# Performance work log

Measured on AMD Instinct MI355X. Metric: run time of the kernel, lower is better.

Reference implementation:

```python
import jax, jax.numpy as jnp
import numpy as np

N_NODES = 8192
N_EDGES = 65536
IN_DIM = 768
HIDDEN = 4096
N_CLASSES = 16


def setup_inputs() -> dict:
    key = jax.random.key(0)
    k1, k2, k3, k4 = jax.random.split(key, 4)
    x = jax.random.normal(k1, (N_NODES, IN_DIM), dtype=jnp.float32)
    edge_index = jax.random.randint(k2, (2, N_EDGES), 0, N_NODES, dtype=jnp.int64)
    # Glorot-ish init scale
    W1 = jax.random.normal(k3, (IN_DIM, HIDDEN), dtype=jnp.float32) * (1.0 / np.sqrt(IN_DIM))
    b1 = jnp.zeros((HIDDEN,), dtype=jnp.float32)
    W2 = jax.random.normal(k4, (HIDDEN, N_CLASSES), dtype=jnp.float32) * (1.0 / np.sqrt(HIDDEN))
    b2 = jnp.zeros((N_CLASSES,), dtype=jnp.float32)
    return {"x": x, "edge_index": edge_index, "W1": W1, "b1": b1, "W2": W2, "b2": b2}


def reference(x, edge_index, W1, b1, W2, b2):
    # GCNConv (PyG defaults): add self-loops, symmetric deg^-1/2 normalization,
    # transform-then-aggregate, plus bias. Then ReLU -> (dropout=identity at
    # inference) -> Linear -> log_softmax.
    N = x.shape[0]
    loops = jnp.arange(N, dtype=edge_index.dtype)
    src = jnp.concatenate([edge_index[0], loops])  # [E+N]
    dst = jnp.concatenate([edge_index[1], loops])  # [E+N]

    h = x @ W1  # [N, HIDDEN] dense GEMM

    deg = jax.ops.segment_sum(jnp.ones_like(dst, dtype=h.dtype), dst, num_segments=N)
    dinv = jnp.where(deg > 0, jax.lax.rsqrt(jnp.maximum(deg, 1e-12)), 0.0)
    norm = dinv[src] * dinv[dst]  # [E+N]

    agg = jax.ops.segment_sum(h[src] * norm[:, None], dst, num_segments=N)  # [N, HIDDEN]
    h = jax.nn.relu(agg + b1)

    logits = h @ W2 + b2  # [N, N_CLASSES]
    return jax.nn.log_softmax(logits, axis=1)
```

## Files before the change

kernel.cpp:

```cpp
#include <hip/hip_runtime.h>

#define N_NODES   8192
#define N_EDGES   65536
#define IN_DIM    768
#define HIDDEN    4096
#define N_CLASSES 16
#define SLOTS     64
#define NSLAB     16

typedef unsigned short ushort_t;
typedef __attribute__((ext_vector_type(8))) short bf16x8;
typedef __attribute__((ext_vector_type(4))) float f32x4;

__device__ __forceinline__ ushort_t f2bf(float f) {
    union { float f; unsigned i; } v; v.f = f;
    unsigned r = v.i + 0x7FFFu + ((v.i >> 16) & 1u);
    return (ushort_t)(r >> 16);
}
__device__ __forceinline__ float bf2f(ushort_t u) {
    union { unsigned i; float f; } v; v.i = ((unsigned)u) << 16; return v.f;
}

#define GLD_LDS16(gp, lp) \
    __builtin_amdgcn_global_load_lds((const __attribute__((address_space(1))) void*)(gp), \
                                     (__attribute__((address_space(3))) void*)(lp), 16, 0, 0)

__device__ __forceinline__ int esrc(const int* ei, int f32mode, int e) {
    return f32mode ? ei[e] : ei[2 * e];
}
__device__ __forceinline__ int edst(const int* ei, int f32mode, int e) {
    return f32mode ? ei[N_EDGES + e] : ei[2 * N_EDGES + 2 * e];
}

__global__ __launch_bounds__(256) void phase1(const float* __restrict__ x,
                                              ushort_t* __restrict__ xbf,
                                              const float* __restrict__ W2,
                                              ushort_t* __restrict__ W2T,
                                              const int* __restrict__ ei,
                                              int* __restrict__ cnt,
                                              int* __restrict__ slots,
                                              int* __restrict__ flag) {
    int b = blockIdx.x, t = threadIdx.x;
    if (b < 16) {
        __shared__ ushort_t ld[16 * 257];
        int k0 = b * 256;
        const float4* src = (const float4*)(W2 + (long)(k0 + t) * N_CLASSES);
        #pragma unroll
        for (int j = 0; j < 4; j++) {
            float4 v = src[j];
            ld[(j * 4 + 0) * 257 + t] = f2bf(v.x);
            ld[(j * 4 + 1) * 257 + t] = f2bf(v.y);
            ld[(j * 4 + 2) * 257 + t] = f2bf(v.z);
            ld[(j * 4 + 3) * 257 + t] = f2bf(v.w);
        }
        __syncthreads();
        #pragma unroll
        for (int c = 0; c < 16; c++)
            W2T[c * HIDDEN + k0 + t] = ld[c * 257 + t];
    } else if (b < 1552) {
        long i = (long)(b - 16) * 1024 + t;
        #pragma unroll
        for (int p = 0; p < 4; p++) {
            float4 v = ((const float4*)x)[i + p * 256];
            ushort4 r = { f2bf(v.x), f2bf(v.y), f2bf(v.z), f2bf(v.w) };
            ((ushort4*)xbf)[i + p * 256] = r;
        }
    } else {
        __shared__ int sv[256];
        int v = 0;
        for (int e = t; e < 4096; e += 256) v |= ei[2 * e + 1];
        sv[t] = v;
        __syncthreads();
        for (int off = 128; off > 0; off >>= 1) {
            if (t < off) sv[t] |= sv[t + off];
            __syncthreads();
        }
        int f = (sv[0] != 0) ? 1 : 0;
        if (b == 1552 && t == 0) *flag = f;
        int e = (b - 1552) * 256 + t;
        int s = esrc(ei, f, e), d = edst(ei, f, e);
        int p = atomicAdd(&cnt[d], 1);
        if (p < SLOTS) slots[d * SLOTS + p] = s;
    }
}

__global__ __launch_bounds__(256) void phase2(const float* __restrict__ W1,
                                              ushort_t* __restrict__ W1T,
                                              const ushort_t* __restrict__ xbf,
                                              const int* __restrict__ cnt,
                                              const int* __restrict__ slots,
                                              const int* __restrict__ ei,
                                              const int* __restrict__ flag,
                                              ushort_t* __restrict__ xagg) {
    int b = blockIdx.x, t = threadIdx.x;
    if (b < 3072) {
        __shared__ ushort_t tile[32][33];
        int n0 = (b & 127) * 32, k0 = (b >> 7) * 32;
        int tx = t & 31, ty = t >> 5;
        #pragma unroll
        for (int j = 0; j < 4; j++) {
            int k = ty * 4 + j;
            tile[k][tx] = f2bf(W1[(k0 + k) * HIDDEN + n0 + tx]);
        }
        __syncthreads();
        #pragma unroll
        for (int j = 0; j < 4; j++) {
            int n = ty * 4 + j;
            W1T[(n0 + n) * IN_DIM + k0 + tx] = tile[tx][n];
        }
        return;
    }
    if (t >= 192) return;
    int w = t >> 6, l = t & 63;
    int d = b - 3072;
    int fo = w * 256 + l * 4;
    int cd = cnt[d];
    float wd = rsqrtf((float)(cd + 1));
    ushort4 sv = *(const ushort4*)(xbf + (long)d * IN_DIM + fo);
    float a0 = wd * bf2f(sv.x), a1 = wd * bf2f(sv.y);
    float a2 = wd * bf2f(sv.z), a3 = wd * bf2f(sv.w);

    if (cd <= SLOTS) {
        const int* sl = slots + d * SLOTS;
        int j = 0;
        for (; j + 4 <= cd; j += 4) {
            int s0 = sl[j], s1 = sl[j + 1], s2 = sl[j + 2], s3 = sl[j + 3];
            float w0 = rsqrtf((float)(cnt[s0] + 1));
            float w1 = rsqrtf((float)(cnt[s1] + 1));
            float w2 = rsqrtf((float)(cnt[s2] + 1));
            float w3 = rsqrtf((float)(cnt[s3] + 1));
            ushort4 v0 = *(const ushort4*)(xbf + (long)s0 * IN_DIM + fo);
            ushort4 v1 = *(const ushort4*)(xbf + (long)s1 * IN_DIM + fo);
            ushort4 v2 = *(const ushort4*)(xbf + (long)s2 * IN_DIM + fo);
            ushort4 v3 = *(const ushort4*)(xbf + (long)s3 * IN_DIM + fo);
            a0 = fmaf(w0, bf2f(v0.x), a0); a1 = fmaf(w0, bf2f(v0.y), a1);
            a2 = fmaf(w0, bf2f(v0.z), a2); a3 = fmaf(w0, bf2f(v0.w), a3);
            a0 = fmaf(w1, bf2f(v1.x), a0); a1 = fmaf(w1, bf2f(v1.y), a1);
            a2 = fmaf(w1, bf2f(v1.z), a2); a3 = fmaf(w1, bf2f(v1.w), a3);
            a0 = fmaf(w2, bf2f(v2.x), a0); a1 = fmaf(w2, bf2f(v2.y), a1);
            a2 = fmaf(w2, bf2f(v2.z), a2); a3 = fmaf(w2, bf2f(v2.w), a3);
            a0 = fmaf(w3, bf2f(v3.x), a0); a1 = fmaf(w3, bf2f(v3.y), a1);
            a2 = fmaf(w3, bf2f(v3.z), a2); a3 = fmaf(w3, bf2f(v3.w), a3);
        }
        for (; j < cd; j++) {
            int s = sl[j];
            float ws = rsqrtf((float)(cnt[s] + 1));
            ushort4 v = *(const ushort4*)(xbf + (long)s * IN_DIM + fo);
            a0 = fmaf(ws, bf2f(v.x), a0); a1 = fmaf(ws, bf2f(v.y), a1);
            a2 = fmaf(ws, bf2f(v.z), a2); a3 = fmaf(ws, bf2f(v.w), a3);
        }
    } else {
        int f = *flag;
        for (int e = 0; e < N_EDGES; e++) {
            if (edst(ei, f, e) == d) {
                int s = esrc(ei, f, e);
                float ws = rsqrtf((float)(cnt[s] + 1));
                ushort4 v = *(const ushort4*)(xbf + (long)s * IN_DIM + fo);
                a0 = fmaf(ws, bf2f(v.x), a0); a1 = fmaf(ws, bf2f(v.y), a1);
                a2 = fmaf(ws, bf2f(v.z), a2); a3 = fmaf(ws, bf2f(v.w), a3);
            }
        }
    }
    ushort4 r = { f2bf(a0 * wd), f2bf(a1 * wd), f2bf(a2 * wd), f2bf(a3 * wd) };
    *(ushort4*)(xagg + (long)d * IN_DIM + fo) = r;
}

#define FENCE() asm volatile("" ::: "memory")
#define BAR()  do { FENCE(); __builtin_amdgcn_s_barrier(); FENCE(); } while (0)
#define VMCNT(n) asm volatile("s_waitcnt vmcnt(" #n ")" ::: "memory")
#define LGKM0()  asm volatile("s_waitcnt lgkmcnt(0)" ::: "memory")
#define PRIO(x)  __builtin_amdgcn_s_setprio(x)

__global__ __launch_bounds__(512, 2) void gemm1_fused(const ushort_t* __restrict__ A,
                                                      const ushort_t* __restrict__ Bt,
                                                      const float* __restrict__ b1,
                                                      const ushort_t* __restrict__ W2T,
                                                      float* __restrict__ part) {
    __shared__ ushort_t lds[65536];
    ushort_t* ldsA = lds;
    ushort_t* ldsB = lds + 32768;

    int t = threadIdx.x;
    int w = t >> 6, l = t & 63;
    int wm = w & 3, wn = w >> 2;
    int q = l >> 4, lm = l & 15;
    int bx = blockIdx.x & 15, by = blockIdx.x >> 4;
    int m0 = by * 256, n0 = bx * 256;

    int srow = t >> 3;
    int sg = (t & 7) ^ (srow & 7);
    const ushort_t* aS = A  + (long)(m0 + srow) * IN_DIM + sg * 8;
    const ushort_t* bS = Bt + (long)(n0 + srow) * IN_DIM + sg * 8;

#define STAGE_A(B_, h, ko) do { \
    GLD_LDS16(aS + (h) * 128 * IN_DIM + (ko),              ldsA + (B_) * 16384 + (h) * 8192 + w * 512); \
    GLD_LDS16(aS + ((h) * 128 + 64) * IN_DIM + (ko),       ldsA + (B_) * 16384 + (h) * 8192 + 4096 + w * 512); \
} while (0)
#define STAGE_B(B_, h, ko) do { \
    GLD_LDS16(bS + (h) * 128 * IN_DIM + (ko),              ldsB + (B_) * 16384 + (h) * 8192 + w * 512); \
    GLD_LDS16(bS + ((h) * 128 + 64) * IN_DIM + (ko),       ldsB + (B_) * 16384 + (h) * 8192 + 4096 + w * 512); \
} while (0)
#define LDA(dst, qm, B_) do { \
    const ushort_t* p_ = ldsA + (B_) * 16384 + (wm * 64 + (qm) * 32 + lm) * 64; \
    int x0_ = ((q) ^ (lm & 7)) * 8, x1_ = ((4 + q) ^ (lm & 7)) * 8; \
    dst[0][0] = *(const bf16x8*)(p_ + x0_);        dst[0][1] = *(const bf16x8*)(p_ + x1_); \
    dst[1][0] = *(const bf16x8*)(p_ + 1024 + x0_); dst[1][1] = *(const bf16x8*)(p_ + 1024 + x1_); \
} while (0)
#define LDB(dst, qn, B_) do { \
    const ushort_t* p_ = ldsB + (B_) * 16384 + (wn * 128 + (qn) * 64 + lm) * 64; \
    int x0_ = ((q) ^ (lm & 7)) * 8, x1_ = ((4 + q) ^ (lm & 7)) * 8; \
    dst[0][0] = *(const bf16x8*)(p_ + x0_);        dst[0][1] = *(const bf16x8*)(p_ + x1_); \
    dst[1][0] = *(const bf16x8*)(p_ + 1024 + x0_); dst[1][1] = *(const bf16x8*)(p_ + 1024 + x1_); \
    dst[2][0] = *(const bf16x8*)(p_ + 2048 + x0_); dst[2][1] = *(const bf16x8*)(p_ + 2048 + x1_); \
    dst[3][0] = *(const bf16x8*)(p_ + 3072 + x0_); dst[3][1] = *(const bf16x8*)(p_ + 3072 + x1_); \
} while (0)
#define MFMAQ(qm, qn, a_, b_) do { \
    _Pragma("unroll") for (int j_ = 0; j_ < 2; j_++) \
    _Pragma("unroll") for (int nt_ = 0; nt_ < 4; nt_++) \
    _Pragma("unroll") for (int mt_ = 0; mt_ < 2; mt_++) \
        acc[(qm) * 2 + mt_][(qn) * 4 + nt_] = __builtin_amdgcn_mfma_f32_16x16x32_bf16( \
            a_[mt_][j_], b_[nt_][j_], acc[(qm) * 2 + mt_][(qn) * 4 + nt_], 0, 0, 0); \
} while (0)

    int kA = 0, kB = 0;
    STAGE_A(0, 0, kA); STAGE_A(0, 1, kA); kA += 64;
    STAGE_B(0, 0, kB); STAGE_B(0, 1, kB); kB += 64;
    STAGE_A(1, 0, kA); STAGE_A(1, 1, kA); kA += 64;

    bf16x8 aq0[2][2], aq1[2][2], bq0[4][2], bq1[4][2];
    f32x4 acc[4][8] = {};

    VMCNT(4);
    BAR();

    #pragma unroll 1
    for (int it = 0; it < 5; ++it) {
        LDA(aq0, 0, 0); LDB(bq0, 0, 0); STAGE_B(1, 0, kB);
        BAR(); LGKM0(); PRIO(1); MFMAQ(0, 0, aq0, bq0); PRIO(0); BAR();
        LDA(aq1, 1, 0); STAGE_B(1, 1, kB); kB += 64;
        BAR(); LGKM0(); PRIO(1); MFMAQ(1, 0, aq1, bq0); PRIO(0); BAR();
        LDB(bq1, 1, 0); STAGE_A(0, 0, kA);
        BAR(); LGKM0(); PRIO(1); MFMAQ(1, 1, aq1, bq1); PRIO(0); BAR();
        STAGE_A(0, 1, kA); kA += 64;
        VMCNT(4);
        BAR(); PRIO(1); MFMAQ(0, 1, aq0, bq1); PRIO(0); BAR();
        LDA(aq0, 0, 1); LDB(bq0, 0, 1); STAGE_B(0, 0, kB);
        BAR(); LGKM0(); PRIO(1); MFMAQ(0, 0, aq0, bq0); PRIO(0); BAR();
        LDA(aq1, 1, 1); STAGE_B(0, 1, kB); kB += 64;
        BAR(); LGKM0(); PRIO(1); MFMAQ(1, 0, aq1, bq0); PRIO(0); BAR();
        LDB(bq1, 1, 1); STAGE_A(1, 0, kA);
        BAR(); LGKM0(); PRIO(1); MFMAQ(1, 1, aq1, bq1); PRIO(0); BAR();
        STAGE_A(1, 1, kA); kA += 64;
        VMCNT(4);
        BAR(); PRIO(1); MFMAQ(0, 1, aq0, bq1); PRIO(0); BAR();
    }
    LDA(aq0, 0, 0); LDB(bq0, 0, 0); STAGE_B(1, 0, kB);
    BAR(); LGKM0(); PRIO(1); MFMAQ(0, 0, aq0, bq0); PRIO(0); BAR();
    LDA(aq1, 1, 0); STAGE_B(1, 1, kB);
    BAR(); LGKM0(); PRIO(1); MFMAQ(1, 0, aq1, bq0); PRIO(0); BAR();
    LDB(bq1, 1, 0);
    BAR(); LGKM0(); PRIO(1); MFMAQ(1, 1, aq1, bq1); PRIO(0); BAR();
    VMCNT(0);
    BAR(); PRIO(1); MFMAQ(0, 1, aq0, bq1); PRIO(0); BAR();
    LDA(aq0, 0, 1); LDB(bq0, 0, 1);
    BAR(); LGKM0(); PRIO(1); MFMAQ(0, 0, aq0, bq0); PRIO(0); BAR();
    LDA(aq1, 1, 1);
    BAR(); LGKM0(); PRIO(1); MFMAQ(1, 0, aq1, bq0); PRIO(0); BAR();
    LDB(bq1, 1, 1);
    BAR(); LGKM0(); PRIO(1); MFMAQ(1, 1, aq1, bq1); PRIO(0); BAR();
    PRIO(1); MFMAQ(0, 1, aq0, bq1); PRIO(0);

    float bias[8];
    #pragma unroll
    for (int ng = 0; ng < 8; ng++) bias[ng] = b1[n0 + wn * 128 + ng * 16 + lm];
    bf16x8 w2f[2][2];
    #pragma unroll
    for (int eh = 0; eh < 2; eh++)
        #pragma unroll
        for (int kk = 0; kk < 2; kk++)
            w2f[eh][kk] = *(const bf16x8*)(W2T + (long)lm * HIDDEN + n0 + wn * 128 + eh * 64 + kk * 32 + q * 8);

    __syncthreads();
    ushort_t* slab = lds + w * 4096;
    f32x4 acc2[4] = {};
    #pragma unroll
    for (int eh = 0; eh < 2; eh++) {
        #pragma unroll
        for (int mg = 0; mg < 4; mg++)
            #pragma unroll
            for (int nt = 0; nt < 4; nt++) {
                int gc = nt * 2 + (lm >> 3);
                #pragma unroll
                for (int rr = 0; rr < 4; rr++) {
                    int row = mg * 16 + q * 4 + rr;
                    float v = acc[mg][eh * 4 + nt][rr] + bias[eh * 4 + nt];
                    v = v > 0.0f ? v : 0.0f;
                    slab[row * 64 + ((gc ^ (row & 7)) * 8) + (lm & 7)] = f2bf(v);
                }
            }
        #pragma unroll
        for (int kk = 0; kk < 2; kk++)
            #pragma unroll
            for (int mt2 = 0; mt2 < 4; mt2++) {
                bf16x8 a2 = *(const bf16x8*)(slab + (mt2 * 16 + lm) * 64 + (((kk * 4 + q) ^ (lm & 7)) * 8));
                acc2[mt2] = __builtin_amdgcn_mfma_f32_16x16x32_bf16(a2, w2f[eh][kk], acc2[mt2], 0, 0, 0);
            }
    }

    __syncthreads();
    float* psum = (float*)lds;
    if (wn == 1) {
        #pragma unroll
        for (int mt2 = 0; mt2 < 4; mt2++)
            #pragma unroll
            for (int rr = 0; rr < 4; rr++)
                psum[(wm * 64 + mt2 * 16 + q * 4 + rr) * 17 + lm] = acc2[mt2][rr];
    }
    __syncthreads();
    if (wn == 0) {
        float* pslab = part + ((long)bx * N_NODES + m0 + wm * 64) * N_CLASSES;
        #pragma unroll
        for (int mt2 = 0; mt2 < 4; mt2++)
            #pragma unroll
            for (int rr = 0; rr < 4; rr++) {
                int row = mt2 * 16 + q * 4 + rr;
                pslab[row * N_CLASSES + lm] = acc2[mt2][rr] + psum[(wm * 64 + row) * 17 + lm];
            }
    }
#undef STAGE_A
#undef STAGE_B
#undef LDA
#undef LDB
#undef MFMAQ
}

__global__ __launch_bounds__(256) void reduce_softmax(const float* __restrict__ part,
                                                      const float* __restrict__ b2,
                                                      float* __restrict__ out) {
    int t = threadIdx.x;
    int row = blockIdx.x * 16 + (t >> 4);
    int cls = t & 15;
    float v = b2[cls];
    #pragma unroll
    for (int s = 0; s < NSLAB; s++)
        v += part[((long)s * N_NODES + row) * N_CLASSES + cls];
    float mx = v;
    #pragma unroll
    for (int off = 1; off < 16; off <<= 1)
        mx = fmaxf(mx, __shfl_xor(mx, off, 64));
    float e = __expf(v - mx);
    float sm = e;
    #pragma unroll
    for (int off = 1; off < 16; off <<= 1)
        sm += __shfl_xor(sm, off, 64);
    out[(long)row * N_CLASSES + cls] = v - mx - __logf(sm);
}


extern "C" void kernel_launch(void* const* d_in, const int* in_sizes, int n_in,
                              void* d_out, int out_size, void* d_ws, size_t ws_size,
                              hipStream_t stream) {
    const float* x  = (const float*)d_in[0];
    const int*   ei = (const int*)d_in[1];
    const float* W1 = (const float*)d_in[2];
    const float* b1 = (const float*)d_in[3];
    const float* W2 = (const float*)d_in[4];
    const float* b2 = (const float*)d_in[5];
    float* out = (float*)d_out;
    char* ws = (char*)d_ws;

    float*    part  = (float*)(ws);
    ushort_t* xagg  = (ushort_t*)(ws + 16777216);
    ushort_t* xbf   = (ushort_t*)(ws + 29360128);
    ushort_t* W1T   = (ushort_t*)(ws + 41943040);
    ushort_t* W2T   = (ushort_t*)(ws + 48234496);
    int*      cnt   = (int*)(ws + 48365568);
    int*      slots = (int*)(ws + 48398336);
    int*      flag  = (int*)(ws + 50495488);

    hipMemsetAsync(cnt, 0, 32768, stream);
    phase1<<<1808, 256, 0, stream>>>(x, xbf, W2, W2T, ei, cnt, slots, flag);
    phase2<<<11264, 256, 0, stream>>>(W1, W1T, xbf, cnt, slots, ei, flag, xagg);
    gemm1_fused<<<(N_NODES / 256) * (HIDDEN / 256), 512, 0, stream>>>(xagg, W1T, b1, W2T, part);
    reduce_softmax<<<N_NODES / 16, 256, 0, stream>>>(part, b2, out);
}
```

Baseline: 159.7 us.

## Move W1 transpose into phase1 and remap gather to one node per wave

Moves the W1 fp32-to-bf16 transpose blocks from phase2 into phase1, so phase2 only does the neighbour aggregation. Phase2 now gives each wave its own destination node and spreads the three 256-feature slices across separate grid passes, which uses all four waves per block instead of idling the fourth. The gather loop is unrolled to 8 neighbours so more independent loads are in flight. The cost is more divergence between waves in a block, since neighbouring nodes have different degrees, and more registers for the deeper unroll.

```diff
diff --git a/kernel.cpp b/kernel.cpp
--- a/kernel.cpp
+++ b/kernel.cpp
@@ -34,6 +34,8 @@
 
 __global__ __launch_bounds__(256) void phase1(const float* __restrict__ x,
                                               ushort_t* __restrict__ xbf,
+                                              const float* __restrict__ W1,
+                                              ushort_t* __restrict__ W1T,
                                               const float* __restrict__ W2,
                                               ushort_t* __restrict__ W2T,
                                               const int* __restrict__ ei,
@@ -65,7 +67,7 @@
             ushort4 r = { f2bf(v.x), f2bf(v.y), f2bf(v.z), f2bf(v.w) };
             ((ushort4*)xbf)[i + p * 256] = r;
         }
-    } else {
+    } else if (b < 1808) {
         __shared__ int sv[256];
         int v = 0;
         for (int e = t; e < 4096; e += 256) v |= ei[2 * e + 1];
@@ -81,83 +83,80 @@
         int s = esrc(ei, f, e), d = edst(ei, f, e);
         int p = atomicAdd(&cnt[d], 1);
         if (p < SLOTS) slots[d * SLOTS + p] = s;
-    }
-}
-
-__global__ __launch_bounds__(256) void phase2(const float* __restrict__ W1,
-                                              ushort_t* __restrict__ W1T,
-                                              const ushort_t* __restrict__ xbf,
+    } else {
+        __shared__ ushort_t tile[32][33];
+        int bt = b - 1808;
+        int n0 = (bt & 127) * 32, k0 = (bt >> 7) * 32;
+        int tx = t & 31, ty = t >> 5;
+        #pragma unroll
+        for (int j = 0; j < 4; j++) {
+            int k = ty * 4 + j;
+            tile[k][tx] = f2bf(W1[(k0 + k) * HIDDEN + n0 + tx]);
+        }
+        __syncthreads();
+        #pragma unroll
+        for (int j = 0; j < 4; j++) {
+            int n = ty * 4 + j;
+            W1T[(n0 + n) * IN_DIM + k0 + tx] = tile[tx][n];
+        }
+    }
+}
+
+__global__ __launch_bounds__(256) void phase2(const ushort_t* __restrict__ xbf,
                                               const int* __restrict__ cnt,
                                               const int* __restrict__ slots,
                                               const int* __restrict__ ei,
                                               const int* __restrict__ flag,
                                               ushort_t* __restrict__ xagg) {
-    int b = blockIdx.x, t = threadIdx.x;
-    if (b < 3072) {
-        __shared__ ushort_t tile[32][33];
-        int n0 = (b & 127) * 32, k0 = (b >> 7) * 32;
-        int tx = t & 31, ty = t >> 5;
-        #pragma unroll
-        for (int j = 0; j < 4; j++) {
-            int k = ty * 4 + j;
-            tile[k][tx] = f2bf(W1[(k0 + k) * HIDDEN + n0 + tx]);
-        }
-        __syncthreads();
-        #pragma unroll
-        for (int j = 0; j < 4; j++) {
-            int n = ty * 4 + j;
-            W1T[(n0 + n) * IN_DIM + k0 + tx] = tile[tx][n];
-        }
-        return;
-    }
-    if (t >= 192) return;
+    int t = threadIdx.x;
     int w = t >> 6, l = t & 63;
-    int d = b - 3072;
-    int fo = w * 256 + l * 4;
+    int b = blockIdx.x;
+    int pass = b >> 11;
+    int d = (b & 2047) * 4 + w;
+    int fo = pass * 256 + l * 4;
     int cd = cnt[d];
     float wd = rsqrtf((float)(cd + 1));
-    ushort4 sv = *(const ushort4*)(xbf + (long)d * IN_DIM + fo);
-    float a0 = wd * bf2f(sv.x), a1 = wd * bf2f(sv.y);
-    float a2 = wd * bf2f(sv.z), a3 = wd * bf2f(sv.w);
-
+    float a0, a1, a2, a3;
+    {
+        ushort4 v = *(const ushort4*)(xbf + (long)d * IN_DIM + fo);
+        a0 = wd * bf2f(v.x); a1 = wd * bf2f(v.y);
+        a2 = wd * bf2f(v.z); a3 = wd * bf2f(v.w);
+    }
     if (cd <= SLOTS) {
         const int* sl = slots + d * SLOTS;
         int j = 0;
-        for (; j + 4 <= cd; j += 4) {
-            int s0 = sl[j], s1 = sl[j + 1], s2 = sl[j + 2], s3 = sl[j + 3];
-            float w0 = rsqrtf((float)(cnt[s0] + 1));
-            float w1 = rsqrtf((float)(cnt[s1] + 1));
-            float w2 = rsqrtf((float)(cnt[s2] + 1));
-            float w3 = rsqrtf((float)(cnt[s3] + 1));
-            ushort4 v0 = *(const ushort4*)(xbf + (long)s0 * IN_DIM + fo);
-            ushort4 v1 = *(const ushort4*)(xbf + (long)s1 * IN_DIM + fo);
-            ushort4 v2 = *(const ushort4*)(xbf + (long)s2 * IN_DIM + fo);
-            ushort4 v3 = *(const ushort4*)(xbf + (long)s3 * IN_DIM + fo);
-            a0 = fmaf(w0, bf2f(v0.x), a0); a1 = fmaf(w0, bf2f(v0.y), a1);
-            a2 = fmaf(w0, bf2f(v0.z), a2); a3 = fmaf(w0, bf2f(v0.w), a3);
-            a0 = fmaf(w1, bf2f(v1.x), a0); a1 = fmaf(w1, bf2f(v1.y), a1);
-            a2 = fmaf(w1, bf2f(v1.z), a2); a3 = fmaf(w1, bf2f(v1.w), a3);
-            a0 = fmaf(w2, bf2f(v2.x), a0); a1 = fmaf(w2, bf2f(v2.y), a1);
-            a2 = fmaf(w2, bf2f(v2.z), a2); a3 = fmaf(w2, bf2f(v2.w), a3);
-            a0 = fmaf(w3, bf2f(v3.x), a0); a1 = fmaf(w3, bf2f(v3.y), a1);
-            a2 = fmaf(w3, bf2f(v3.z), a2); a3 = fmaf(w3, bf2f(v3.w), a3);
+        for (; j + 8 <= cd; j += 8) {
+            int s[8]; float ws[8]; ushort4 v[8];
+            #pragma unroll
+            for (int k = 0; k < 8; k++) s[k] = sl[j + k];
+            #pragma unroll
+            for (int k = 0; k < 8; k++) ws[k] = rsqrtf((float)(cnt[s[k]] + 1));
+            #pragma unroll
+            for (int k = 0; k < 8; k++) v[k] = *(const ushort4*)(xbf + (long)s[k] * IN_DIM + fo);
+            #pragma unroll
+            for (int k = 0; k < 8; k++) {
+                a0 = fmaf(ws[k], bf2f(v[k].x), a0);
+                a1 = fmaf(ws[k], bf2f(v[k].y), a1);
+                a2 = fmaf(ws[k], bf2f(v[k].z), a2);
+                a3 = fmaf(ws[k], bf2f(v[k].w), a3);
+            }
         }
         for (; j < cd; j++) {
             int s = sl[j];
-            float ws = rsqrtf((float)(cnt[s] + 1));
+            float wsv = rsqrtf((float)(cnt[s] + 1));
             ushort4 v = *(const ushort4*)(xbf + (long)s * IN_DIM + fo);
-            a0 = fmaf(ws, bf2f(v.x), a0); a1 = fmaf(ws, bf2f(v.y), a1);
-            a2 = fmaf(ws, bf2f(v.z), a2); a3 = fmaf(ws, bf2f(v.w), a3);
+            a0 = fmaf(wsv, bf2f(v.x), a0); a1 = fmaf(wsv, bf2f(v.y), a1);
+            a2 = fmaf(wsv, bf2f(v.z), a2); a3 = fmaf(wsv, bf2f(v.w), a3);
         }
     } else {
         int f = *flag;
         for (int e = 0; e < N_EDGES; e++) {
             if (edst(ei, f, e) == d) {
                 int s = esrc(ei, f, e);
-                float ws = rsqrtf((float)(cnt[s] + 1));
+                float wsv = rsqrtf((float)(cnt[s] + 1));
                 ushort4 v = *(const ushort4*)(xbf + (long)s * IN_DIM + fo);
-                a0 = fmaf(ws, bf2f(v.x), a0); a1 = fmaf(ws, bf2f(v.y), a1);
-                a2 = fmaf(ws, bf2f(v.z), a2); a3 = fmaf(ws, bf2f(v.w), a3);
+                a0 = fmaf(wsv, bf2f(v.x), a0); a1 = fmaf(wsv, bf2f(v.y), a1);
+                a2 = fmaf(wsv, bf2f(v.z), a2); a3 = fmaf(wsv, bf2f(v.w), a3);
             }
         }
     }
@@ -379,8 +378,8 @@
     int*      flag  = (int*)(ws + 50495488);
 
     hipMemsetAsync(cnt, 0, 32768, stream);
-    phase1<<<1808, 256, 0, stream>>>(x, xbf, W2, W2T, ei, cnt, slots, flag);
-    phase2<<<11264, 256, 0, stream>>>(W1, W1T, xbf, cnt, slots, ei, flag, xagg);
+    phase1<<<4880, 256, 0, stream>>>(x, xbf, W1, W1T, W2, W2T, ei, cnt, slots, flag);
+    phase2<<<6144, 256, 0, stream>>>(xbf, cnt, slots, ei, flag, xagg);
     gemm1_fused<<<(N_NODES / 256) * (HIDDEN / 256), 512, 0, stream>>>(xagg, W1T, b1, W2T, part);
     reduce_softmax<<<N_NODES / 16, 256, 0, stream>>>(part, b2, out);
 }
```

Result: slower. 164.5 us (+3.0%).

## Restructure phase2: wider transpose tiles, one wave per node, interleaved block roles

Applied to the files above, without the earlier changes.

The W1 transpose now uses 64x64 tiles with float4 loads and 16-byte bf16 stores instead of 32x32 scalar tiles. Aggregation blocks now handle four nodes each, one per wave, and each lane covers 12 features, so all 256 threads are used and the per-edge slot and degree lookups are spread over more loads. Transpose and aggregation blocks are interleaved one in four, so both kinds of work run concurrently across the grid, which shrinks from 11264 to 3072 blocks. This raises register pressure per thread, and the 64x72 shared tile is declared for every block.

```diff
diff --git a/kernel.cpp b/kernel.cpp
--- a/kernel.cpp
+++ b/kernel.cpp
@@ -84,6 +84,15 @@
     }
 }
 
+#define ACC3(W_, v0_, v1_, v2_) do { \
+    a[0] = fmaf(W_, bf2f(v0_.x), a[0]); a[1]  = fmaf(W_, bf2f(v0_.y), a[1]); \
+    a[2] = fmaf(W_, bf2f(v0_.z), a[2]); a[3]  = fmaf(W_, bf2f(v0_.w), a[3]); \
+    a[4] = fmaf(W_, bf2f(v1_.x), a[4]); a[5]  = fmaf(W_, bf2f(v1_.y), a[5]); \
+    a[6] = fmaf(W_, bf2f(v1_.z), a[6]); a[7]  = fmaf(W_, bf2f(v1_.w), a[7]); \
+    a[8] = fmaf(W_, bf2f(v2_.x), a[8]); a[9]  = fmaf(W_, bf2f(v2_.y), a[9]); \
+    a[10] = fmaf(W_, bf2f(v2_.z), a[10]); a[11] = fmaf(W_, bf2f(v2_.w), a[11]); \
+} while (0)
+
 __global__ __launch_bounds__(256) void phase2(const float* __restrict__ W1,
                                               ushort_t* __restrict__ W1T,
                                               const ushort_t* __restrict__ xbf,
@@ -92,34 +101,49 @@
                                               const int* __restrict__ ei,
                                               const int* __restrict__ flag,
                                               ushort_t* __restrict__ xagg) {
+    __shared__ ushort_t tile[64][72];
     int b = blockIdx.x, t = threadIdx.x;
-    if (b < 3072) {
-        __shared__ ushort_t tile[32][33];
-        int n0 = (b & 127) * 32, k0 = (b >> 7) * 32;
-        int tx = t & 31, ty = t >> 5;
-        #pragma unroll
-        for (int j = 0; j < 4; j++) {
-            int k = ty * 4 + j;
-            tile[k][tx] = f2bf(W1[(k0 + k) * HIDDEN + n0 + tx]);
+    if ((b & 3) == 3) {
+        int bt = b >> 2;
+        int k0 = (bt >> 6) * 64, n0 = (bt & 63) * 64;
+        #pragma unroll
+        for (int p = 0; p < 4; p++) {
+            int k = p * 16 + (t >> 4);
+            int c = (t & 15) * 4;
+            float4 v = *(const float4*)(W1 + (long)(k0 + k) * HIDDEN + n0 + c);
+            ushort4 r = { f2bf(v.x), f2bf(v.y), f2bf(v.z), f2bf(v.w) };
+            *(ushort4*)&tile[k][c] = r;
         }
         __syncthreads();
-        #pragma unroll
-        for (int j = 0; j < 4; j++) {
-            int n = ty * 4 + j;
-            W1T[(n0 + n) * IN_DIM + k0 + tx] = tile[tx][n];
-        }
+        int n = t >> 2, kk0 = (t & 3) * 16;
+        ushort_t buf[16];
+        #pragma unroll
+        for (int kk = 0; kk < 16; kk++) buf[kk] = tile[kk0 + kk][n];
+        ushort_t* dst = W1T + (long)(n0 + n) * IN_DIM + k0 + kk0;
+        *(bf16x8*)(dst)     = *(bf16x8*)&buf[0];
+        *(bf16x8*)(dst + 8) = *(bf16x8*)&buf[8];
         return;
     }
-    if (t >= 192) return;
+    int idx = (b >> 2) * 3 + (b & 3);
+    if (idx >= 2048) return;
     int w = t >> 6, l = t & 63;
-    int d = b - 3072;
-    int fo = w * 256 + l * 4;
+    int d = idx * 4 + w;
+    int fo = l * 4;
     int cd = cnt[d];
     float wd = rsqrtf((float)(cd + 1));
-    ushort4 sv = *(const ushort4*)(xbf + (long)d * IN_DIM + fo);
-    float a0 = wd * bf2f(sv.x), a1 = wd * bf2f(sv.y);
-    float a2 = wd * bf2f(sv.z), a3 = wd * bf2f(sv.w);
-
+    float a[12];
+    {
+        const ushort_t* pr = xbf + (long)d * IN_DIM + fo;
+        ushort4 v0 = *(const ushort4*)(pr);
+        ushort4 v1 = *(const ushort4*)(pr + 256);
+        ushort4 v2 = *(const ushort4*)(pr + 512);
+        a[0] = wd * bf2f(v0.x); a[1]  = wd * bf2f(v0.y);
+        a[2] = wd * bf2f(v0.z); a[3]  = wd * bf2f(v0.w);
+        a[4] = wd * bf2f(v1.x); a[5]  = wd * bf2f(v1.y);
+        a[6] = wd * bf2f(v1.z); a[7]  = wd * bf2f(v1.w);
+        a[8] = wd * bf2f(v2.x); a[9]  = wd * bf2f(v2.y);
+        a[10] = wd * bf2f(v2.z); a[11] = wd * bf2f(v2.w);
+    }
     if (cd <= SLOTS) {
         const int* sl = slots + d * SLOTS;
         int j = 0;
@@ -129,40 +153,45 @@
             float w1 = rsqrtf((float)(cnt[s1] + 1));
             float w2 = rsqrtf((float)(cnt[s2] + 1));
             float w3 = rsqrtf((float)(cnt[s3] + 1));
-            ushort4 v0 = *(const ushort4*)(xbf + (long)s0 * IN_DIM + fo);
-            ushort4 v1 = *(const ushort4*)(xbf + (long)s1 * IN_DIM + fo);
-            ushort4 v2 = *(const ushort4*)(xbf + (long)s2 * IN_DIM + fo);
-            ushort4 v3 = *(const ushort4*)(xbf + (long)s3 * IN_DIM + fo);
-            a0 = fmaf(w0, bf2f(v0.x), a0); a1 = fmaf(w0, bf2f(v0.y), a1);
-            a2 = fmaf(w0, bf2f(v0.z), a2); a3 = fmaf(w0, bf2f(v0.w), a3);
-            a0 = fmaf(w1, bf2f(v1.x), a0); a1 = fmaf(w1, bf2f(v1.y), a1);
-            a2 = fmaf(w1, bf2f(v1.z), a2); a3 = fmaf(w1, bf2f(v1.w), a3);
-            a0 = fmaf(w2, bf2f(v2.x), a0); a1 = fmaf(w2, bf2f(v2.y), a1);
-            a2 = fmaf(w2, bf2f(v2.z), a2); a3 = fmaf(w2, bf2f(v2.w), a3);
-            a0 = fmaf(w3, bf2f(v3.x), a0); a1 = fmaf(w3, bf2f(v3.y), a1);
-            a2 = fmaf(w3, bf2f(v3.z), a2); a3 = fmaf(w3, bf2f(v3.w), a3);
+            const ushort_t* p0 = xbf + (long)s0 * IN_DIM + fo;
+            const ushort_t* p1 = xbf + (long)s1 * IN_DIM + fo;
+            const ushort_t* p2 = xbf + (long)s2 * IN_DIM + fo;
+            const ushort_t* p3 = xbf + (long)s3 * IN_DIM + fo;
+            ushort4 v00 = *(const ushort4*)(p0), v01 = *(const ushort4*)(p0 + 256), v02 = *(const ushort4*)(p0 + 512);
+            ushort4 v10 = *(const ushort4*)(p1), v11 = *(const ushort4*)(p1 + 256), v12 = *(const ushort4*)(p1 + 512);
+            ushort4 v20 = *(const ushort4*)(p2), v21 = *(const ushort4*)(p2 + 256), v22 = *(const ushort4*)(p2 + 512);
+            ushort4 v30 = *(const ushort4*)(p3), v31 = *(const ushort4*)(p3 + 256), v32 = *(const ushort4*)(p3 + 512);
+            ACC3(w0, v00, v01, v02);
+            ACC3(w1, v10, v11, v12);
+            ACC3(w2, v20, v21, v22);
+            ACC3(w3, v30, v31, v32);
         }
         for (; j < cd; j++) {
             int s = sl[j];
-            float ws = rsqrtf((float)(cnt[s] + 1));
-            ushort4 v = *(const ushort4*)(xbf + (long)s * IN_DIM + fo);
-            a0 = fmaf(ws, bf2f(v.x), a0); a1 = fmaf(ws, bf2f(v.y), a1);
-            a2 = fmaf(ws, bf2f(v.z), a2); a3 = fmaf(ws, bf2f(v.w), a3);
+            float wsv = rsqrtf((float)(cnt[s] + 1));
+            const ushort_t* pp = xbf + (long)s * IN_DIM + fo;
+            ushort4 u0 = *(const ushort4*)(pp), u1 = *(const ushort4*)(pp + 256), u2 = *(const ushort4*)(pp + 512);
+            ACC3(wsv, u0, u1, u2);
         }
     } else {
         int f = *flag;
         for (int e = 0; e < N_EDGES; e++) {
             if (edst(ei, f, e) == d) {
                 int s = esrc(ei, f, e);
-                float ws = rsqrtf((float)(cnt[s] + 1));
-                ushort4 v = *(const ushort4*)(xbf + (long)s * IN_DIM + fo);
-                a0 = fmaf(ws, bf2f(v.x), a0); a1 = fmaf(ws, bf2f(v.y), a1);
-                a2 = fmaf(ws, bf2f(v.z), a2); a3 = fmaf(ws, bf2f(v.w), a3);
+                float wsv = rsqrtf((float)(cnt[s] + 1));
+                const ushort_t* pp = xbf + (long)s * IN_DIM + fo;
+                ushort4 u0 = *(const ushort4*)(pp), u1 = *(const ushort4*)(pp + 256), u2 = *(const ushort4*)(pp + 512);
+                ACC3(wsv, u0, u1, u2);
             }
         }
     }
-    ushort4 r = { f2bf(a0 * wd), f2bf(a1 * wd), f2bf(a2 * wd), f2bf(a3 * wd) };
-    *(ushort4*)(xagg + (long)d * IN_DIM + fo) = r;
+    ushort_t* po = xagg + (long)d * IN_DIM + fo;
+    ushort4 r0 = { f2bf(a[0] * wd), f2bf(a[1] * wd), f2bf(a[2] * wd), f2bf(a[3] * wd) };
+    ushort4 r1 = { f2bf(a[4] * wd), f2bf(a[5] * wd), f2bf(a[6] * wd), f2bf(a[7] * wd) };
+    ushort4 r2 = { f2bf(a[8] * wd), f2bf(a[9] * wd), f2bf(a[10] * wd), f2bf(a[11] * wd) };
+    *(ushort4*)(po) = r0;
+    *(ushort4*)(po + 256) = r1;
+    *(ushort4*)(po + 512) = r2;
 }
 
 #define FENCE() asm volatile("" ::: "memory")
@@ -380,7 +409,7 @@
 
     hipMemsetAsync(cnt, 0, 32768, stream);
     phase1<<<1808, 256, 0, stream>>>(x, xbf, W2, W2T, ei, cnt, slots, flag);
-    phase2<<<11264, 256, 0, stream>>>(W1, W1T, xbf, cnt, slots, ei, flag, xagg);
+    phase2<<<3072, 256, 0, stream>>>(W1, W1T, xbf, cnt, slots, ei, flag, xagg);
     gemm1_fused<<<(N_NODES / 256) * (HIDDEN / 256), 512, 0, stream>>>(xagg, W1T, b1, W2T, part);
     reduce_softmax<<<N_NODES / 16, 256, 0, stream>>>(part, b2, out);
 }
```

Result: no change. 160.1 us (+0.2%).
